# Optimization experiments

Hardware: AMD Instinct MI355X
Metric: run time of the kernel (lower is better)

Reference implementation:

```python
import jax, jax.numpy as jnp
import numpy as np

TEMPERATURE = 1.0  # module's set_temperature value; mode=False path: out = x + attn_out * temperature


def setup_inputs() -> dict:
    key = jax.random.key(0)
    ks = jax.random.split(key, 7)
    B, C, H, W = 4, 256, 64, 64
    Cqk = C // 8
    s = 0.02
    return {
        "x": jax.random.normal(ks[0], (B, C, H, W), dtype=jnp.float32),
        "Wq": jax.random.normal(ks[1], (Cqk, C), dtype=jnp.float32) * s,
        "bq": jax.random.normal(ks[2], (Cqk,), dtype=jnp.float32) * s,
        "Wk": jax.random.normal(ks[3], (Cqk, C), dtype=jnp.float32) * s,
        "bk": jax.random.normal(ks[4], (Cqk,), dtype=jnp.float32) * s,
        "Wv": jax.random.normal(ks[5], (C, C), dtype=jnp.float32) * s,
        "bv": jax.random.normal(ks[6], (C,), dtype=jnp.float32) * s,
    }


def reference(x, Wq, bq, Wk, bk, Wv, bv):
    B, C, H, W = x.shape
    N = H * W
    xf = x.reshape(B, C, N)                      # flatten spatial -> tokens
    # 1x1 convs == pointwise linear over channels
    q = jnp.einsum('oc,bcn->bno', Wq, xf) + bq            # [B, N, Cqk]
    k = jnp.einsum('oc,bcn->bon', Wk, xf) + bk[:, None]   # [B, Cqk, N]
    attn = jax.nn.softmax(jnp.einsum('bno,bom->bnm', q, k), axis=-1)  # [B, N, N]
    v = jnp.einsum('oc,bcn->bon', Wv, xf) + bv[:, None]   # [B, C, N]
    # torch: bmm(value, attn^T) -> out[b,c,m] = sum_n v[b,c,n] * attn[b,m,n]
    out = jnp.einsum('bcn,bmn->bcm', v, attn).reshape(B, C, H, W)
    return x + out * TEMPERATURE
```

## Files before the change

### kernel.cpp

```cpp
#include <hip/hip_runtime.h>

#define BATCH 4
#define CH    256
#define NTOK  4096
#define DQK   32

typedef __attribute__((ext_vector_type(4))) float  f32x4;
typedef __attribute__((ext_vector_type(2))) float  f32x2;
typedef __attribute__((ext_vector_type(8))) __bf16 bf16x8;
typedef __attribute__((ext_vector_type(2))) unsigned int u32x2;
typedef __attribute__((ext_vector_type(4))) unsigned int u32x4;

static __device__ __forceinline__ unsigned short f2bf(float f) {
    unsigned int u = __builtin_bit_cast(unsigned int, f);
    unsigned int r = u + 0x7FFFu + ((u >> 16) & 1u);
    return (unsigned short)(r >> 16);
}
static __device__ __forceinline__ unsigned int pack2(float a, float b) {
    return (unsigned int)f2bf(a) | ((unsigned int)f2bf(b) << 16);
}

__global__ __launch_bounds__(256)
void wconv(const float* __restrict__ Wq, const float* __restrict__ Wk,
           const float* __restrict__ Wv, unsigned short* __restrict__ Wbf,
           unsigned int* __restrict__ Mk)
{
    if (blockIdx.x == 0 && threadIdx.x < BATCH) Mk[threadIdx.x] = 0u;
    const int id = (blockIdx.x * 256 + threadIdx.x) * 4;
    const int r  = id >> 8;
    const int c  = id & 255;
    const float* src = (r < 32) ? (Wq + r * 256 + c)
                     : (r < 64) ? (Wk + (r - 32) * 256 + c)
                                : (Wv + (size_t)(r - 64) * 256 + c);
    float v0 = src[0], v1 = src[1], v2 = src[2], v3 = src[3];
    u32x2 p = {pack2(v0, v1), pack2(v2, v3)};
    *reinterpret_cast<u32x2*>(Wbf + id) = p;
}

__global__ __launch_bounds__(256, 4)
void qkv_proj(const float* __restrict__ x,
              const float* __restrict__ pbq, const float* __restrict__ pbk,
              const float* __restrict__ pbv,
              const unsigned short* __restrict__ Wbf,
              unsigned short* __restrict__ Qh,
              unsigned short* __restrict__ Kh,
              unsigned short* __restrict__ Vh,
              unsigned int* __restrict__ Mk)
{
    const int t    = threadIdx.x;
    const int wave = t >> 6;
    const int lane = t & 63;
    const int low  = lane & 15;
    const int quad = lane >> 4;
    const int tok0 = blockIdx.x * 16;
    const int b    = tok0 >> 12;
    const int nl0  = tok0 & (NTOK - 1);

    __shared__ unsigned short ob[256 * 24];

    f32x4 acc[5];
    #pragma unroll
    for (int j = 0; j < 5; ++j) {
        const int rtg = wave * 5 + j;
        float bb = (rtg < 2) ? pbq[rtg * 16 + low]
                 : (rtg < 4) ? pbk[(rtg - 2) * 16 + low]
                             : pbv[(rtg - 4) * 16 + low];
        f32x4 z = {bb, bb, bb, bb};
        acc[j] = z;
    }

    const float* xb = x + (size_t)b * CH * NTOK + nl0 + low;

    #pragma unroll
    for (int k0 = 0; k0 < 8; ++k0) {
        const int cbase = k0 * 32 + quad * 8;
        float xv[8];
        #pragma unroll
        for (int e = 0; e < 8; ++e)
            xv[e] = xb[(size_t)(cbase + e) * NTOK];
        u32x4 ap = {pack2(xv[0], xv[1]), pack2(xv[2], xv[3]),
                    pack2(xv[4], xv[5]), pack2(xv[6], xv[7])};
        const bf16x8 af = __builtin_bit_cast(bf16x8, ap);
        #pragma unroll
        for (int j = 0; j < 5; ++j) {
            const int rtg = wave * 5 + j;
            const bf16x8 bf = *reinterpret_cast<const bf16x8*>(
                Wbf + (size_t)(rtg * 16 + low) * 256 + k0 * 32 + quad * 8);
            acc[j] = __builtin_amdgcn_mfma_f32_16x16x32_bf16(af, bf, acc[j], 0, 0, 0);
        }
    }

    #pragma unroll
    for (int j = 0; j < 5; ++j) {
        const int rtg = wave * 5 + j;
        if (rtg < 4) {
            unsigned short* dst = (rtg < 2) ? Qh : Kh;
            const int wr = (rtg & 1) * 16 + low;
            #pragma unroll
            for (int reg = 0; reg < 4; ++reg) {
                const int token = tok0 + quad * 4 + reg;
                dst[(size_t)token * DQK + wr] = f2bf(acc[j][reg]);
            }
        }
    }
    if (wave == 0) {
        f32x4 kk = acc[2] * acc[2] + acc[3] * acc[3];
        #pragma unroll
        for (int mask = 1; mask <= 8; mask <<= 1)
            #pragma unroll
            for (int reg = 0; reg < 4; ++reg)
                kk[reg] += __shfl_xor(kk[reg], mask);
        if (low == 0) {
            #pragma unroll
            for (int reg = 0; reg < 4; ++reg)
                atomicMax(&Mk[b], __builtin_bit_cast(unsigned int, kk[reg]));
        }
    }

    #pragma unroll
    for (int j = 0; j < 5; ++j) {
        const int rtg = wave * 5 + j;
        if (rtg >= 4) {
            const int c = (rtg - 4) * 16 + low;
            #pragma unroll
            for (int reg = 0; reg < 4; ++reg)
                ob[c * 24 + quad * 4 + reg] = f2bf(acc[j][reg]);
        }
    }
    __syncthreads();
    {
        const unsigned int* obd = (const unsigned int*)ob;
        const int h = t & 1;
        #pragma unroll
        for (int pass = 0; pass < 2; ++pass) {
            const int c = (t >> 1) + pass * 128;
            const u32x4 v = *reinterpret_cast<const u32x4*>(obd + c * 12 + h * 4);
            *reinterpret_cast<u32x4*>(
                Vh + ((size_t)b * CH + c) * NTOK + nl0 + h * 8) = v;
        }
    }
}

__global__ __launch_bounds__(512, 2)
void attn(const float* __restrict__ x,
          const unsigned short* __restrict__ Qh,
          const unsigned short* __restrict__ Kh,
          const unsigned short* __restrict__ Vh,
          const unsigned int* __restrict__ Mk,
          float* __restrict__ out)
{
    const int t    = threadIdx.x;
    const int wave = t >> 6;
    const int kg   = wave & 3;
    const int ch   = wave >> 2;
    const int lane = t & 63;
    const int low  = lane & 15;
    const int quad = lane >> 4;

    const int beta = blockIdx.x;
    const int b    = (beta & 7) >> 1;
    const int q0   = (((beta >> 3) * 2) + (beta & 1)) * 64;

    __shared__ float smem[18432 + 256];
    unsigned int* Pbase = (unsigned int*)smem;
    float* lbuf = smem + 18432;

    const float LOG2E = 1.44269504088896f;

    bf16x8 qfrag[2];
    float  m2[2];
    {
        const float M2 = __builtin_bit_cast(float, Mk[b]);
        #pragma unroll
        for (int j = 0; j < 2; ++j) {
            const int qs = 2 * ch + j;
            qfrag[j] = *reinterpret_cast<const bf16x8*>(
                Qh + (size_t)(b * NTOK + q0 + qs * 16 + low) * DQK + quad * 8);
            float qn2 = 0.f;
            #pragma unroll
            for (int e = 0; e < 8; ++e) {
                float qv = (float)qfrag[j][e];
                qn2 += qv * qv;
            }
            qn2 += __shfl_xor(qn2, 16);
            qn2 += __shfl_xor(qn2, 32);
            m2[j] = __builtin_sqrtf(qn2 * M2) * (1.02f * LOG2E);
        }
    }

    f32x4 acc[4][8];
    #pragma unroll
    for (int qs = 0; qs < 4; ++qs)
        #pragma unroll
        for (int ct = 0; ct < 8; ++ct) { f32x4 z = {0.f,0.f,0.f,0.f}; acc[qs][ct] = z; }
    float l_s[2] = {0.f, 0.f};

    const unsigned short* Kb = Kh + (size_t)b * NTOK * DQK;
    const unsigned short* Vb = Vh + (size_t)b * CH * NTOK;

    #define S_PHASE(ii, buf)                                                    \
    {                                                                           \
        const int n0s = ((ii) * 4 + kg) * 64;                                   \
        bf16x8 kf[4];                                                           \
        _Pragma("unroll")                                                       \
        for (int kt = 0; kt < 4; ++kt)                                          \
            kf[kt] = *reinterpret_cast<const bf16x8*>(                          \
                Kb + (size_t)(n0s + kt * 16 + low) * DQK + quad * 8);           \
        _Pragma("unroll")                                                       \
        for (int j = 0; j < 2; ++j) {                                           \
            const int qs = 2 * ch + j;                                          \
            f32x4 S[4];                                                         \
            _Pragma("unroll")                                                   \
            for (int kt = 0; kt < 4; ++kt) {                                    \
                f32x4 z = {0.f,0.f,0.f,0.f};                                    \
                S[kt] = __builtin_amdgcn_mfma_f32_16x16x32_bf16(kf[kt],         \
                            qfrag[j], z, 0, 0, 0);                              \
            }                                                                   \
            float sum = 0.f;                                                    \
            unsigned int* pq = Pbase + (buf) * 9216 + kg * 2304                 \
                               + (qs * 16 + low) * 36 + quad * 2;               \
            _Pragma("unroll")                                                   \
            for (int kt = 0; kt < 4; ++kt) {                                    \
                float p0 = __builtin_amdgcn_exp2f(S[kt][0] * LOG2E - m2[j]);    \
                float p1 = __builtin_amdgcn_exp2f(S[kt][1] * LOG2E - m2[j]);    \
                float p2 = __builtin_amdgcn_exp2f(S[kt][2] * LOG2E - m2[j]);    \
                float p3 = __builtin_amdgcn_exp2f(S[kt][3] * LOG2E - m2[j]);    \
                sum += (p0 + p1) + (p2 + p3);                                   \
                u32x2 w2 = {pack2(p0, p1), pack2(p2, p3)};                      \
                *reinterpret_cast<u32x2*>(pq + kt * 8) = w2;                    \
            }                                                                   \
            l_s[j] += sum;                                                      \
        }                                                                       \
    }

    S_PHASE(0, 0)

    for (int i = 0; i < 16; ++i) {
        __syncthreads();

        if (i < 15) S_PHASE(i + 1, (i + 1) & 1)

        {
            const int n0 = (i * 4 + kg) * 64;
            const unsigned short* Phh =
                (const unsigned short*)(Pbase + (i & 1) * 9216);
            #pragma unroll
            for (int s = 0; s < 2; ++s) {
                bf16x8 pf[4];
                #pragma unroll
                for (int qs = 0; qs < 4; ++qs)
                    pf[qs] = *reinterpret_cast<const bf16x8*>(
                        Phh + kg * 4608 + (qs * 16 + low) * 72 + s * 32 + quad * 8);
                #pragma unroll
                for (int ct = 0; ct < 8; ++ct) {
                    const bf16x8 vf = *reinterpret_cast<const bf16x8*>(
                        Vb + (size_t)(ch * 128 + ct * 16 + low) * NTOK
                           + n0 + s * 32 + quad * 8);
                    #pragma unroll
                    for (int qs = 0; qs < 4; ++qs)
                        acc[qs][ct] = __builtin_amdgcn_mfma_f32_16x16x32_bf16(
                            vf, pf[qs], acc[qs][ct], 0, 0, 0);
                }
            }
        }
    }
    #undef S_PHASE

    #pragma unroll
    for (int j = 0; j < 2; ++j) {
        l_s[j] += __shfl_xor(l_s[j], 16);
        l_s[j] += __shfl_xor(l_s[j], 32);
    }
    if (quad == 0) {
        #pragma unroll
        for (int j = 0; j < 2; ++j)
            lbuf[kg * 64 + (2 * ch + j) * 16 + low] = l_s[j];
    }

    const int q = t & 63;
    const int u = t >> 6;
    float invl = 0.f;
    for (int rd = 0; rd < 8; ++rd) {
        #pragma unroll
        for (int qs = 0; qs < 4; ++qs) {
            float* sl = smem + wave * 1408 + (qs * 16 + low) * 22 + quad * 4;
            f32x2 lo = {acc[qs][rd][0], acc[qs][rd][1]};
            f32x2 hi = {acc[qs][rd][2], acc[qs][rd][3]};
            *reinterpret_cast<f32x2*>(sl)     = lo;
            *reinterpret_cast<f32x2*>(sl + 2) = hi;
        }
        __syncthreads();
        if (rd == 0)
            invl = 1.0f / (((lbuf[q] + lbuf[64 + q]) + (lbuf[128 + q] + lbuf[192 + q])));

        #pragma unroll
        for (int p = 0; p < 4; ++p) {
            const int half = p >> 1;
            const int c15  = u * 2 + (p & 1);
            const int wb   = half * 4;
            float O = (smem[(wb + 0) * 1408 + q * 22 + c15]
                     + smem[(wb + 1) * 1408 + q * 22 + c15])
                    + (smem[(wb + 2) * 1408 + q * 22 + c15]
                     + smem[(wb + 3) * 1408 + q * 22 + c15]);
            const int c = half * 128 + rd * 16 + c15;
            const size_t idx = (size_t)(b * CH + c) * NTOK + q0 + q;
            out[idx] = x[idx] + O * invl;
        }
        __syncthreads();
    }
}

extern "C" void kernel_launch(void* const* d_in, const int* in_sizes, int n_in,
                              void* d_out, int out_size, void* d_ws, size_t ws_size,
                              hipStream_t stream) {
    const float* x  = (const float*)d_in[0];
    const float* Wq = (const float*)d_in[1];
    const float* bq = (const float*)d_in[2];
    const float* Wk = (const float*)d_in[3];
    const float* bk = (const float*)d_in[4];
    const float* Wv = (const float*)d_in[5];
    const float* bv = (const float*)d_in[6];
    float* out = (float*)d_out;

    unsigned short* Qh  = (unsigned short*)d_ws;
    unsigned short* Kh  = Qh  + (size_t)BATCH * NTOK * DQK;
    unsigned short* Vh  = Kh  + (size_t)BATCH * NTOK * DQK;
    unsigned short* Wbf = Vh  + (size_t)BATCH * CH * NTOK;
    unsigned int*   Mk  = (unsigned int*)(Wbf + 320 * 256);

    wconv<<<dim3(80), dim3(256), 0, stream>>>(Wq, Wk, Wv, Wbf, Mk);
    qkv_proj<<<dim3(1024), dim3(256), 0, stream>>>(x, bq, bk, bv, Wbf,
                                                   Qh, Kh, Vh, Mk);
    attn<<<dim3(256), dim3(512), 0, stream>>>(x, Qh, Kh, Vh, Mk, out);
}
```

Before: 242.3 us.

## Make P tiles wave-private to drop per-iteration barrier, use hardware bf16 pack

Each wave now computes the softmax probabilities for all 64 queries of its key chunk itself, writing them into a private LDS region. This removes the __syncthreads in the main loop. The cost is that each (kg) pair of waves duplicates the QK^T and exp work, and the P buffer in LDS doubles in size. The change also swaps the manual bf16 rounding for v_cvt_pk_bf16_f32 and raises wave priority around the PV MFMA block.

New measurement: 222.5 us. 8.2% less time.

```diff
diff --git a/kernel.cpp b/kernel.cpp
--- a/kernel.cpp
+++ b/kernel.cpp
@@ -18,6 +18,11 @@
 }
 static __device__ __forceinline__ unsigned int pack2(float a, float b) {
     return (unsigned int)f2bf(a) | ((unsigned int)f2bf(b) << 16);
+}
+static __device__ __forceinline__ unsigned int cvt_pk_bf16(float a, float b) {
+    unsigned int r;
+    asm("v_cvt_pk_bf16_f32 %0, %1, %2" : "=v"(r) : "v"(a), "v"(b));
+    return r;
 }
 
 __global__ __launch_bounds__(256)
@@ -78,8 +83,8 @@
         #pragma unroll
         for (int e = 0; e < 8; ++e)
             xv[e] = xb[(size_t)(cbase + e) * NTOK];
-        u32x4 ap = {pack2(xv[0], xv[1]), pack2(xv[2], xv[3]),
-                    pack2(xv[4], xv[5]), pack2(xv[6], xv[7])};
+        u32x4 ap = {cvt_pk_bf16(xv[0], xv[1]), cvt_pk_bf16(xv[2], xv[3]),
+                    cvt_pk_bf16(xv[4], xv[5]), cvt_pk_bf16(xv[6], xv[7])};
         const bf16x8 af = __builtin_bit_cast(bf16x8, ap);
         #pragma unroll
         for (int j = 0; j < 5; ++j) {
@@ -161,21 +166,20 @@
     const int b    = (beta & 7) >> 1;
     const int q0   = (((beta >> 3) * 2) + (beta & 1)) * 64;
 
-    __shared__ float smem[18432 + 256];
+    __shared__ float smem[36864 + 256];
     unsigned int* Pbase = (unsigned int*)smem;
-    float* lbuf = smem + 18432;
+    float* lbuf = smem + 36864;
 
     const float LOG2E = 1.44269504088896f;
 
-    bf16x8 qfrag[2];
-    float  m2[2];
+    bf16x8 qfrag[4];
+    float  m2[4];
     {
         const float M2 = __builtin_bit_cast(float, Mk[b]);
         #pragma unroll
-        for (int j = 0; j < 2; ++j) {
-            const int qs = 2 * ch + j;
+        for (int j = 0; j < 4; ++j) {
             qfrag[j] = *reinterpret_cast<const bf16x8*>(
-                Qh + (size_t)(b * NTOK + q0 + qs * 16 + low) * DQK + quad * 8);
+                Qh + (size_t)(b * NTOK + q0 + j * 16 + low) * DQK + quad * 8);
             float qn2 = 0.f;
             #pragma unroll
             for (int e = 0; e < 8; ++e) {
@@ -193,7 +197,7 @@
     for (int qs = 0; qs < 4; ++qs)
         #pragma unroll
         for (int ct = 0; ct < 8; ++ct) { f32x4 z = {0.f,0.f,0.f,0.f}; acc[qs][ct] = z; }
-    float l_s[2] = {0.f, 0.f};
+    float l_s[4] = {0.f, 0.f, 0.f, 0.f};
 
     const unsigned short* Kb = Kh + (size_t)b * NTOK * DQK;
     const unsigned short* Vb = Vh + (size_t)b * CH * NTOK;
@@ -207,8 +211,7 @@
             kf[kt] = *reinterpret_cast<const bf16x8*>(                          \
                 Kb + (size_t)(n0s + kt * 16 + low) * DQK + quad * 8);           \
         _Pragma("unroll")                                                       \
-        for (int j = 0; j < 2; ++j) {                                           \
-            const int qs = 2 * ch + j;                                          \
+        for (int j = 0; j < 4; ++j) {                                           \
             f32x4 S[4];                                                         \
             _Pragma("unroll")                                                   \
             for (int kt = 0; kt < 4; ++kt) {                                    \
@@ -217,8 +220,8 @@
                             qfrag[j], z, 0, 0, 0);                              \
             }                                                                   \
             float sum = 0.f;                                                    \
-            unsigned int* pq = Pbase + (buf) * 9216 + kg * 2304                 \
-                               + (qs * 16 + low) * 36 + quad * 2;               \
+            unsigned int* pq = Pbase + (buf) * 18432 + wave * 2304              \
+                               + (j * 16 + low) * 36 + quad * 2;                \
             _Pragma("unroll")                                                   \
             for (int kt = 0; kt < 4; ++kt) {                                    \
                 float p0 = __builtin_amdgcn_exp2f(S[kt][0] * LOG2E - m2[j]);    \
@@ -226,7 +229,7 @@
                 float p2 = __builtin_amdgcn_exp2f(S[kt][2] * LOG2E - m2[j]);    \
                 float p3 = __builtin_amdgcn_exp2f(S[kt][3] * LOG2E - m2[j]);    \
                 sum += (p0 + p1) + (p2 + p3);                                   \
-                u32x2 w2 = {pack2(p0, p1), pack2(p2, p3)};                      \
+                u32x2 w2 = {cvt_pk_bf16(p0, p1), cvt_pk_bf16(p2, p3)};          \
                 *reinterpret_cast<u32x2*>(pq + kt * 8) = w2;                    \
             }                                                                   \
             l_s[j] += sum;                                                      \
@@ -236,21 +239,20 @@
     S_PHASE(0, 0)
 
     for (int i = 0; i < 16; ++i) {
-        __syncthreads();
-
         if (i < 15) S_PHASE(i + 1, (i + 1) & 1)
 
         {
             const int n0 = (i * 4 + kg) * 64;
             const unsigned short* Phh =
-                (const unsigned short*)(Pbase + (i & 1) * 9216);
+                (const unsigned short*)(Pbase + (i & 1) * 18432 + wave * 2304);
+            __builtin_amdgcn_s_setprio(1);
             #pragma unroll
             for (int s = 0; s < 2; ++s) {
                 bf16x8 pf[4];
                 #pragma unroll
                 for (int qs = 0; qs < 4; ++qs)
                     pf[qs] = *reinterpret_cast<const bf16x8*>(
-                        Phh + kg * 4608 + (qs * 16 + low) * 72 + s * 32 + quad * 8);
+                        Phh + (qs * 16 + low) * 72 + s * 32 + quad * 8);
                 #pragma unroll
                 for (int ct = 0; ct < 8; ++ct) {
                     const bf16x8 vf = *reinterpret_cast<const bf16x8*>(
@@ -262,20 +264,24 @@
                             vf, pf[qs], acc[qs][ct], 0, 0, 0);
                 }
             }
+            __builtin_amdgcn_s_setprio(0);
         }
     }
     #undef S_PHASE
 
     #pragma unroll
-    for (int j = 0; j < 2; ++j) {
+    for (int j = 0; j < 4; ++j) {
         l_s[j] += __shfl_xor(l_s[j], 16);
         l_s[j] += __shfl_xor(l_s[j], 32);
     }
     if (quad == 0) {
         #pragma unroll
-        for (int j = 0; j < 2; ++j)
-            lbuf[kg * 64 + (2 * ch + j) * 16 + low] = l_s[j];
-    }
+        for (int jj = 0; jj < 2; ++jj) {
+            const int qs = 2 * ch + jj;
+            lbuf[kg * 64 + qs * 16 + low] = l_s[qs];
+        }
+    }
+    __syncthreads();
 
     const int q = t & 63;
     const int u = t >> 6;
```
